# Performance work log

Hardware: AMD Instinct MI355X
Metric: run time of the kernel (lower is better)

## Reference

```python
import jax, jax.numpy as jnp
import numpy as np

B, L, C, H = 256, 256, 512, 512
MOG_ITERS = 5

def _xavier(key, shape):
    fan_in, fan_out = shape[0], shape[1]
    lim = jnp.sqrt(6.0 / (fan_in + fan_out))
    return jax.random.uniform(key, shape, jnp.float32, -lim, lim)

def setup_inputs() -> dict:
    key = jax.random.key(0)
    ks = jax.random.split(key, 7)
    x = jax.random.normal(ks[0], (B, L, C), jnp.float32)
    # Linear weights stored as (in, out); torch Linear computes x @ W.T + b, identical math.
    Wih_w = _xavier(ks[1], (C, 4 * H)); Wih_b = jnp.zeros((4 * H,), jnp.float32)
    Wmx_w = _xavier(ks[2], (C, H));     Wmx_b = jnp.zeros((H,), jnp.float32)
    Wmh_w = _xavier(ks[3], (H, H));     Wmh_b = jnp.zeros((H,), jnp.float32)
    Whm_w = _xavier(ks[4], (H, 4 * H)); Whm_b = jnp.zeros((4 * H,), jnp.float32)
    Q = _xavier(ks[5], (H, C))  # ht @ Q -> (B, C)
    R = _xavier(ks[6], (C, H))  # xt @ R -> (B, H)
    return {"x": x, "Wih_w": Wih_w, "Wih_b": Wih_b, "Wmx_w": Wmx_w, "Wmx_b": Wmx_b,
            "Wmh_w": Wmh_w, "Wmh_b": Wmh_b, "Whm_w": Whm_w, "Whm_b": Whm_b, "Q": Q, "R": R}

def reference(x, Wih_w, Wih_b, Wmx_w, Wmx_b, Wmh_w, Wmh_b, Whm_w, Whm_b, Q, R):
    batch = x.shape[0]
    h0 = jnp.zeros((batch, H), x.dtype)
    c0 = jnp.zeros((batch, H), x.dtype)

    def step(carry, xt):
        ht, Ct = carry
        # Mogrify: odd iters update xt, even iters update ht
        for i in range(1, MOG_ITERS + 1):
            if i % 2 == 0:
                ht = 2.0 * jax.nn.sigmoid(xt @ R) * ht
            else:
                xt = 2.0 * jax.nn.sigmoid(ht @ Q) * xt
        mt = (xt @ Wmx_w + Wmx_b) + (ht @ Wmh_w + Wmh_b)
        gates = (xt @ Wih_w + Wih_b) + (mt @ Whm_w + Whm_b)
        ingate, forgetgate, cellgate, outgate = jnp.split(gates, 4, axis=1)
        ft = jax.nn.sigmoid(forgetgate)
        it = jax.nn.sigmoid(ingate)
        cand = jnp.tanh(cellgate)
        ot = jax.nn.sigmoid(outgate)
        Ct = ft * Ct + it * cand
        ht = ot * jnp.tanh(Ct)
        return (ht, Ct), ht

    xs = jnp.swapaxes(x, 0, 1)  # (L, B, C)
    _, hs = jax.lax.scan(step, (h0, c0), xs)
    return jnp.swapaxes(hs, 0, 1)  # (B, L, H)
```

## Files before the change

### kernel.cpp

```cpp
#include <hip/hip_runtime.h>
#include <hip/hip_bf16.h>
#include <cmath>

typedef __attribute__((ext_vector_type(8))) short short8;
typedef __attribute__((ext_vector_type(4))) float f32x4;
typedef __attribute__((ext_vector_type(2))) float f32x2;
typedef __attribute__((ext_vector_type(4))) unsigned int u32x4;

__device__ inline float bf2f(ushort u) {
    unsigned v = (unsigned)u << 16; float f; __builtin_memcpy(&f, &v, 4); return f;
}
__device__ inline ushort f2bf(float f) {
    __hip_bfloat16 h = __float2bfloat16(f); ushort u; __builtin_memcpy(&u, &h, 2); return u;
}
__device__ inline float sigf(float z) { return 1.f / (1.f + expf(-z)); }

__device__ __forceinline__ void agst32(void* p, unsigned v) {
    __hip_atomic_store((unsigned*)p, v, __ATOMIC_RELAXED, __HIP_MEMORY_SCOPE_AGENT);
}

#define BB 256
#define LL 256
#define HH 512
#define G4 2048

__device__ __forceinline__ unsigned swz(unsigned row, unsigned byteInRow) {
    return (row * 1024u + byteInRow) ^ ((row & 7u) << 4);
}

__device__ __forceinline__ void stage_A16(const ushort* Ag, int r0, ushort* Ast, int tid) {
    const char* src = (const char*)(Ag + (size_t)(r0 + (tid >> 4)) * HH + (tid & 15) * 32);
    u32x4 v0, v1, v2, v3;
    asm volatile(
        "global_load_dwordx4 %0, %4, off sc0 sc1\n\t"
        "global_load_dwordx4 %1, %4, off offset:16 sc0 sc1\n\t"
        "global_load_dwordx4 %2, %4, off offset:32 sc0 sc1\n\t"
        "global_load_dwordx4 %3, %4, off offset:48 sc0 sc1\n\t"
        "s_waitcnt vmcnt(0)"
        : "=&v"(v0), "=&v"(v1), "=&v"(v2), "=&v"(v3) : "v"(src) : "memory");
    unsigned row = (unsigned)(tid >> 4), b = (unsigned)((tid & 15) * 64);
    *(u32x4*)((char*)Ast + swz(row, b))      = v0;
    *(u32x4*)((char*)Ast + swz(row, b + 16)) = v1;
    *(u32x4*)((char*)Ast + swz(row, b + 32)) = v2;
    *(u32x4*)((char*)Ast + swz(row, b + 48)) = v3;
}

__device__ __forceinline__ void rb_arrive(unsigned* slots, int sub, unsigned epoch) {
    asm volatile("s_waitcnt vmcnt(0)" ::: "memory");
    __syncthreads();
    if (threadIdx.x == 0)
        __hip_atomic_store(slots + sub, epoch, __ATOMIC_RELAXED, __HIP_MEMORY_SCOPE_AGENT);
}
__device__ __forceinline__ void rb_wait(unsigned* slots, unsigned epoch) {
    if (threadIdx.x < 16)
        while (__hip_atomic_load(slots + threadIdx.x, __ATOMIC_RELAXED,
                                 __HIP_MEMORY_SCOPE_AGENT) < epoch)
            __builtin_amdgcn_s_sleep(1);
    __syncthreads();
}


__global__ __launch_bounds__(256) void init_state(ushort* hp) {
    int i = blockIdx.x * 256 + threadIdx.x;
    hp[i] = 0;
}

__global__ __launch_bounds__(256) void transpose_f32_bf16(
    const float* __restrict__ in, ushort* __restrict__ out, int K, int N)
{
    __shared__ float tile[32][33];
    int tx = threadIdx.x & 31, ty = threadIdx.x >> 5;
    int bk = blockIdx.x * 32, bn = blockIdx.y * 32;
    #pragma unroll
    for (int i = 0; i < 32; i += 8)
        tile[ty + i][tx] = in[(size_t)(bk + ty + i) * N + (bn + tx)];
    __syncthreads();
    #pragma unroll
    for (int i = 0; i < 32; i += 8)
        out[(size_t)(bn + ty + i) * K + (bk + tx)] = f2bf(tile[tx][ty + i]);
}

__global__ __launch_bounds__(256) void combine_w(
    const float* __restrict__ base, const float* __restrict__ A,
    const float* __restrict__ Bm, float* __restrict__ out, int use_base)
{
    int n  = blockIdx.x * 256 + threadIdx.x;
    int k0 = blockIdx.y * 8;
    float acc[8];
    #pragma unroll
    for (int r = 0; r < 8; ++r)
        acc[r] = use_base ? base[(size_t)(k0 + r) * G4 + n] : 0.f;
    for (int m = 0; m < 512; ++m) {
        float bv = Bm[(size_t)m * G4 + n];
        #pragma unroll
        for (int r = 0; r < 8; ++r)
            acc[r] = fmaf(A[(size_t)(k0 + r) * 512 + m], bv, acc[r]);
    }
    #pragma unroll
    for (int r = 0; r < 8; ++r) out[(size_t)(k0 + r) * G4 + n] = acc[r];
}

__global__ __launch_bounds__(256) void bias_g_kernel(
    const float* __restrict__ Wih_b, const float* __restrict__ Whm_b,
    const float* __restrict__ Wmx_b, const float* __restrict__ Wmh_b,
    const float* __restrict__ Whm, float* __restrict__ bias_g)
{
    int n = blockIdx.x * 256 + threadIdx.x;
    float acc = Wih_b[n] + Whm_b[n];
    for (int m = 0; m < 512; ++m)
        acc = fmaf(Wmx_b[m] + Wmh_b[m], Whm[(size_t)m * G4 + n], acc);
    bias_g[n] = acc;
}


__device__ __forceinline__ void mog_stage_p(
    const ushort* Ast,
    const ushort* Wlds,
    ushort (*myBuf)[32], ushort* __restrict__ outG,
    const float* __restrict__ xscale, float (*pbuf)[16][16],
    int r0, int cs, int t, int tid)
{
    int lane = tid & 63, wave = tid >> 6;
    int lr = lane & 15, lk = lane >> 4;
    int ct = wave & 1, kh = wave >> 1;
    int colloc = ct * 16 + lr;

    float xs[4];
    if (xscale != nullptr && kh == 0) {
        #pragma unroll
        for (int r = 0; r < 4; ++r)
            xs[r] = xscale[((size_t)(r0 + lk * 4 + r) * LL + t) * HH + cs * 32 + colloc];
    }

    f32x4 acc = {0.f, 0.f, 0.f, 0.f};
    #pragma unroll
    for (int kk = 0; kk < 8; ++kk) {
        short8 a = *(const short8*)((const char*)Ast +
                     swz((unsigned)lr, (unsigned)(kh * 512 + kk * 64 + lk * 16)));
        short8 b = *(const short8*)((const char*)Wlds +
                     swz((unsigned)colloc, (unsigned)(kh * 512 + kk * 64 + lk * 16)));
        acc = __builtin_amdgcn_mfma_f32_16x16x32_bf16(a, b, acc, 0, 0, 0);
    }

    if (kh == 1) {
        #pragma unroll
        for (int r = 0; r < 4; ++r) pbuf[ct][lk * 4 + r][lr] = acc[r];
    }
    __syncthreads();
    if (kh == 0) {
        #pragma unroll
        for (int r = 0; r < 4; ++r) {
            float v = acc[r] + pbuf[ct][lk * 4 + r][lr];
            float sc = (xscale != nullptr) ? xs[r] : bf2f(myBuf[lk * 4 + r][colloc]);
            myBuf[lk * 4 + r][colloc] = f2bf(2.f * sigf(v) * sc);
        }
    }
    __syncthreads();
    {
        int row = tid >> 4, c2 = tid & 15;
        unsigned v = *(const unsigned*)&myBuf[row][c2 * 2];
        agst32((char*)outG + (((size_t)(r0 + row)) * HH + cs * 32 + c2 * 2) * 2, v);
    }
}

__global__ __launch_bounds__(256) void moglstm_persistent(
    const float* __restrict__ x,
    const ushort* __restrict__ QT, const ushort* __restrict__ RT,
    const ushort* __restrict__ W1T, const ushort* __restrict__ W2T,
    const float* __restrict__ biasg,
    ushort* __restrict__ hp, ushort* __restrict__ xa, ushort* __restrict__ hb1,
    ushort* __restrict__ xb, ushort* __restrict__ hb2, ushort* __restrict__ xc,
    float* __restrict__ out, unsigned* __restrict__ flags)
{
    __shared__ ushort QTs[32 * 512];
    __shared__ ushort RTs[32 * 512];
    __shared__ ushort Ast[16 * 512];
    __shared__ float  pbuf[2][16][16];
    __shared__ ushort myX[16][32];
    __shared__ ushort myH[16][32];
    __shared__ float  gbuf[4][16][32];

    int tid = threadIdx.x;
    int rb = blockIdx.x >> 4, cs = blockIdx.x & 15;
    int r0 = rb * 16;
    int lane = tid & 63, wave = tid >> 6;
    int lr = lane & 15, lk = lane >> 4;

    #pragma unroll
    for (int i = 0; i < 8; ++i) {
        int ch = i * 256 + tid, col = ch >> 6, kc = ch & 63;
        *(u32x4*)((char*)QTs + swz((unsigned)col, (unsigned)(kc * 16))) =
            *(const u32x4*)(QT + (size_t)(cs * 32 + col) * HH + kc * 8);
        *(u32x4*)((char*)RTs + swz((unsigned)col, (unsigned)(kc * 16))) =
            *(const u32x4*)(RT + (size_t)(cs * 32 + col) * HH + kc * 8);
    }
    ((unsigned*)myH)[tid] = 0;
    float Creg0 = 0.f, Creg1 = 0.f;
    __syncthreads();

    unsigned* slots = flags + rb * 16;

    for (int t = 0; t < LL; ++t) {
        unsigned ep = (unsigned)t * 6u;

        stage_A16(hp, r0, Ast, tid); __syncthreads();
        mog_stage_p(Ast, QTs, myX, xa, x, pbuf, r0, cs, t, tid);
        rb_arrive(slots, cs, ep + 1); rb_wait(slots, ep + 1);
        stage_A16(xa, r0, Ast, tid); __syncthreads();
        mog_stage_p(Ast, RTs, myH, hb1, nullptr, pbuf, r0, cs, t, tid);
        rb_arrive(slots, cs, ep + 2); rb_wait(slots, ep + 2);
        stage_A16(hb1, r0, Ast, tid); __syncthreads();
        mog_stage_p(Ast, QTs, myX, xb, nullptr, pbuf, r0, cs, t, tid);
        rb_arrive(slots, cs, ep + 3); rb_wait(slots, ep + 3);
        stage_A16(xb, r0, Ast, tid); __syncthreads();
        mog_stage_p(Ast, RTs, myH, hb2, nullptr, pbuf, r0, cs, t, tid);
        rb_arrive(slots, cs, ep + 4); rb_wait(slots, ep + 4);

        stage_A16(hb2, r0, Ast, tid); __syncthreads();
        mog_stage_p(Ast, QTs, myX, xc, nullptr, pbuf, r0, cs, t, tid);
        rb_arrive(slots, cs, ep + 5);

        int q = wave;
        f32x4 acc0 = {0,0,0,0}, acc1 = {0,0,0,0};
        {
            const short8* B0 = (const short8*)(W2T + (size_t)(q * 512 + cs * 32 + lr) * HH);
            const short8* B1 = (const short8*)(W2T + (size_t)(q * 512 + cs * 32 + 16 + lr) * HH);
            #pragma unroll
            for (int kk = 0; kk < 16; ++kk) {
                short8 a = *(const short8*)((const char*)Ast +
                             swz((unsigned)lr, (unsigned)(kk * 64 + lk * 16)));
                acc0 = __builtin_amdgcn_mfma_f32_16x16x32_bf16(a, B0[kk * 4 + lk], acc0, 0, 0, 0);
                acc1 = __builtin_amdgcn_mfma_f32_16x16x32_bf16(a, B1[kk * 4 + lk], acc1, 0, 0, 0);
            }
        }
        rb_wait(slots, ep + 5);

        stage_A16(xc, r0, Ast, tid); __syncthreads();
        {
            const short8* B0 = (const short8*)(W1T + (size_t)(q * 512 + cs * 32 + lr) * HH);
            const short8* B1 = (const short8*)(W1T + (size_t)(q * 512 + cs * 32 + 16 + lr) * HH);
            #pragma unroll
            for (int kk = 0; kk < 16; ++kk) {
                short8 a = *(const short8*)((const char*)Ast +
                             swz((unsigned)lr, (unsigned)(kk * 64 + lk * 16)));
                acc0 = __builtin_amdgcn_mfma_f32_16x16x32_bf16(a, B0[kk * 4 + lk], acc0, 0, 0, 0);
                acc1 = __builtin_amdgcn_mfma_f32_16x16x32_bf16(a, B1[kk * 4 + lk], acc1, 0, 0, 0);
            }
        }
        {
            float b0 = biasg[q * 512 + cs * 32 + lr];
            float b1 = biasg[q * 512 + cs * 32 + 16 + lr];
            #pragma unroll
            for (int r = 0; r < 4; ++r) {
                gbuf[q][lk * 4 + r][lr]      = acc0[r] + b0;
                gbuf[q][lk * 4 + r][16 + lr] = acc1[r] + b1;
            }
        }
        __syncthreads();
        {
            int row = tid >> 4, c2 = tid & 15;
            int colg = cs * 32 + c2 * 2;
            float i0 = sigf(gbuf[0][row][c2 * 2]),      f0 = sigf(gbuf[1][row][c2 * 2]);
            float g0 = tanhf(gbuf[2][row][c2 * 2]),     o0 = sigf(gbuf[3][row][c2 * 2]);
            Creg0 = f0 * Creg0 + i0 * g0;
            float h0v = o0 * tanhf(Creg0);
            float i1 = sigf(gbuf[0][row][c2 * 2 + 1]),  f1 = sigf(gbuf[1][row][c2 * 2 + 1]);
            float g1 = tanhf(gbuf[2][row][c2 * 2 + 1]), o1 = sigf(gbuf[3][row][c2 * 2 + 1]);
            Creg1 = f1 * Creg1 + i1 * g1;
            float h1v = o1 * tanhf(Creg1);
            f32x2 hv2 = {h0v, h1v};
            *(f32x2*)(out + ((size_t)(r0 + row) * LL + t) * HH + colg) = hv2;
            unsigned hu = (unsigned)f2bf(h0v) | ((unsigned)f2bf(h1v) << 16);
            agst32((char*)hp + (((size_t)(r0 + row)) * HH + colg) * 2, hu);
            *(unsigned*)&myH[row][c2 * 2] = hu;
        }
        rb_arrive(slots, cs, ep + 6); rb_wait(slots, ep + 6);
    }
}

extern "C" void kernel_launch(void* const* d_in, const int* in_sizes, int n_in,
                              void* d_out, int out_size, void* d_ws, size_t ws_size,
                              hipStream_t stream)
{
    const float* x     = (const float*)d_in[0];
    const float* Wih_w = (const float*)d_in[1];
    const float* Wih_b = (const float*)d_in[2];
    const float* Wmx_w = (const float*)d_in[3];
    const float* Wmx_b = (const float*)d_in[4];
    const float* Wmh_w = (const float*)d_in[5];
    const float* Wmh_b = (const float*)d_in[6];
    const float* Whm_w = (const float*)d_in[7];
    const float* Whm_b = (const float*)d_in[8];
    const float* Q     = (const float*)d_in[9];
    const float* R     = (const float*)d_in[10];
    float* out = (float*)d_out;

    char* ws = (char*)d_ws;
    ushort* QT   = (ushort*)ws;               ws += (size_t)512 * 512 * 2;
    ushort* RT   = (ushort*)ws;               ws += (size_t)512 * 512 * 2;
    ushort* W1T  = (ushort*)ws;               ws += (size_t)G4  * 512 * 2;
    ushort* W2T  = (ushort*)ws;               ws += (size_t)G4  * 512 * 2;
    float*  biasg= (float*)ws;                ws += (size_t)G4 * 4;
    ushort* xa   = (ushort*)ws;               ws += (size_t)BB * HH * 2;
    ushort* hb1  = (ushort*)ws;               ws += (size_t)BB * HH * 2;
    ushort* xb   = (ushort*)ws;               ws += (size_t)BB * HH * 2;
    ushort* hb2  = (ushort*)ws;               ws += (size_t)BB * HH * 2;
    ushort* xc   = (ushort*)ws;               ws += (size_t)BB * HH * 2;
    ushort* hp   = (ushort*)ws;               ws += (size_t)BB * HH * 2;
    float*  Wtmp = (float*)ws;                ws += (size_t)512 * G4 * 4;

    unsigned* flags = (unsigned*)Wtmp;

    init_state<<<512, 256, 0, stream>>>(hp);
    transpose_f32_bf16<<<dim3(16, 16), 256, 0, stream>>>(Q, QT, 512, 512);
    transpose_f32_bf16<<<dim3(16, 16), 256, 0, stream>>>(R, RT, 512, 512);
    combine_w<<<dim3(8, 64), 256, 0, stream>>>(Wih_w, Wmx_w, Whm_w, Wtmp, 1);
    transpose_f32_bf16<<<dim3(16, 64), 256, 0, stream>>>(Wtmp, W1T, 512, G4);
    combine_w<<<dim3(8, 64), 256, 0, stream>>>(nullptr, Wmh_w, Whm_w, Wtmp, 0);
    transpose_f32_bf16<<<dim3(16, 64), 256, 0, stream>>>(Wtmp, W2T, 512, G4);
    bias_g_kernel<<<8, 256, 0, stream>>>(Wih_b, Whm_b, Wmx_b, Wmh_b, Whm_w, biasg);
    hipMemsetAsync(flags, 0, (size_t)16 * 16 * sizeof(unsigned), stream);

    moglstm_persistent<<<256, 256, 0, stream>>>(x, QT, RT, W1T, W2T, biasg,
                                                hp, xa, hb1, xb, hb2, xc, out, flags);
}
```

Measured before the change: 7.258 ms.

## Replace block-wide barriers with per-wave flags and per-slice polling

Swaps the row-block barrier for per-wave epoch flags. Before, one thread published a block flag after a __syncthreads and 16 threads polled every peer before a second __syncthreads. Now each wave publishes its own flag once its stores drain, and each lane polls only the four wave flags of the producer block whose slice it is about to load. This removes a block barrier and all-to-all waiting from each of the six dependent stages per timestep. The cost is four times as many flags and more polling traffic, plus a risk of LDS reuse hazards where the removed barriers used to order Ast reads and writes.

```diff
diff --git a/kernel.cpp b/kernel.cpp
--- a/kernel.cpp
+++ b/kernel.cpp
@@ -28,8 +28,24 @@
     return (row * 1024u + byteInRow) ^ ((row & 7u) << 4);
 }
 
-__device__ __forceinline__ void stage_A16(const ushort* Ag, int r0, ushort* Ast, int tid) {
-    const char* src = (const char*)(Ag + (size_t)(r0 + (tid >> 4)) * HH + (tid & 15) * 32);
+__device__ __forceinline__ void arrive_wave(unsigned* fl, int cs, unsigned epoch, int tid) {
+    asm volatile("s_waitcnt vmcnt(0)" ::: "memory");
+    if ((tid & 63) == 0)
+        __hip_atomic_store(fl + cs * 4 + (tid >> 6), epoch,
+                           __ATOMIC_RELAXED, __HIP_MEMORY_SCOPE_AGENT);
+}
+
+__device__ __forceinline__ void stage_poll(
+    const ushort* __restrict__ Ag, int r0, ushort* Ast,
+    unsigned* __restrict__ fl, unsigned epoch, int tid)
+{
+    int w = tid >> 6, l = tid & 63;
+    int p = 4 * w + (l >> 4);
+    int row = l & 15;
+    unsigned* myf = fl + p * 4 + (l & 3);
+    while (__hip_atomic_load(myf, __ATOMIC_RELAXED, __HIP_MEMORY_SCOPE_AGENT) < epoch)
+        __builtin_amdgcn_s_sleep(1);
+    const char* src = (const char*)(Ag + (size_t)(r0 + row) * HH + p * 32);
     u32x4 v0, v1, v2, v3;
     asm volatile(
         "global_load_dwordx4 %0, %4, off sc0 sc1\n\t"
@@ -38,25 +54,11 @@
         "global_load_dwordx4 %3, %4, off offset:48 sc0 sc1\n\t"
         "s_waitcnt vmcnt(0)"
         : "=&v"(v0), "=&v"(v1), "=&v"(v2), "=&v"(v3) : "v"(src) : "memory");
-    unsigned row = (unsigned)(tid >> 4), b = (unsigned)((tid & 15) * 64);
-    *(u32x4*)((char*)Ast + swz(row, b))      = v0;
-    *(u32x4*)((char*)Ast + swz(row, b + 16)) = v1;
-    *(u32x4*)((char*)Ast + swz(row, b + 32)) = v2;
-    *(u32x4*)((char*)Ast + swz(row, b + 48)) = v3;
-}
-
-__device__ __forceinline__ void rb_arrive(unsigned* slots, int sub, unsigned epoch) {
-    asm volatile("s_waitcnt vmcnt(0)" ::: "memory");
-    __syncthreads();
-    if (threadIdx.x == 0)
-        __hip_atomic_store(slots + sub, epoch, __ATOMIC_RELAXED, __HIP_MEMORY_SCOPE_AGENT);
-}
-__device__ __forceinline__ void rb_wait(unsigned* slots, unsigned epoch) {
-    if (threadIdx.x < 16)
-        while (__hip_atomic_load(slots + threadIdx.x, __ATOMIC_RELAXED,
-                                 __HIP_MEMORY_SCOPE_AGENT) < epoch)
-            __builtin_amdgcn_s_sleep(1);
-    __syncthreads();
+    unsigned b = (unsigned)(p * 64);
+    *(u32x4*)((char*)Ast + swz((unsigned)row, b))      = v0;
+    *(u32x4*)((char*)Ast + swz((unsigned)row, b + 16)) = v1;
+    *(u32x4*)((char*)Ast + swz((unsigned)row, b + 32)) = v2;
+    *(u32x4*)((char*)Ast + swz((unsigned)row, b + 48)) = v3;
 }
 
 
@@ -113,9 +115,8 @@
 }
 
 
-__device__ __forceinline__ void mog_stage_p(
-    const ushort* Ast,
-    const ushort* Wlds,
+__device__ __forceinline__ void mog_compute(
+    const ushort* Ast, const ushort* Wlds,
     ushort (*myBuf)[32], ushort* __restrict__ outG,
     const float* __restrict__ xscale, float (*pbuf)[16][16],
     int r0, int cs, int t, int tid)
@@ -198,27 +199,26 @@
     float Creg0 = 0.f, Creg1 = 0.f;
     __syncthreads();
 
-    unsigned* slots = flags + rb * 16;
+    unsigned* fl = flags + rb * 64;
 
     for (int t = 0; t < LL; ++t) {
         unsigned ep = (unsigned)t * 6u;
 
-        stage_A16(hp, r0, Ast, tid); __syncthreads();
-        mog_stage_p(Ast, QTs, myX, xa, x, pbuf, r0, cs, t, tid);
-        rb_arrive(slots, cs, ep + 1); rb_wait(slots, ep + 1);
-        stage_A16(xa, r0, Ast, tid); __syncthreads();
-        mog_stage_p(Ast, RTs, myH, hb1, nullptr, pbuf, r0, cs, t, tid);
-        rb_arrive(slots, cs, ep + 2); rb_wait(slots, ep + 2);
-        stage_A16(hb1, r0, Ast, tid); __syncthreads();
-        mog_stage_p(Ast, QTs, myX, xb, nullptr, pbuf, r0, cs, t, tid);
-        rb_arrive(slots, cs, ep + 3); rb_wait(slots, ep + 3);
-        stage_A16(xb, r0, Ast, tid); __syncthreads();
-        mog_stage_p(Ast, RTs, myH, hb2, nullptr, pbuf, r0, cs, t, tid);
-        rb_arrive(slots, cs, ep + 4); rb_wait(slots, ep + 4);
-
-        stage_A16(hb2, r0, Ast, tid); __syncthreads();
-        mog_stage_p(Ast, QTs, myX, xc, nullptr, pbuf, r0, cs, t, tid);
-        rb_arrive(slots, cs, ep + 5);
+        stage_poll(hp, r0, Ast, fl, ep, tid); __syncthreads();
+        mog_compute(Ast, QTs, myX, xa, x, pbuf, r0, cs, t, tid);
+        arrive_wave(fl, cs, ep + 1, tid);
+        stage_poll(xa, r0, Ast, fl, ep + 1, tid); __syncthreads();
+        mog_compute(Ast, RTs, myH, hb1, nullptr, pbuf, r0, cs, t, tid);
+        arrive_wave(fl, cs, ep + 2, tid);
+        stage_poll(hb1, r0, Ast, fl, ep + 2, tid); __syncthreads();
+        mog_compute(Ast, QTs, myX, xb, nullptr, pbuf, r0, cs, t, tid);
+        arrive_wave(fl, cs, ep + 3, tid);
+        stage_poll(xb, r0, Ast, fl, ep + 3, tid); __syncthreads();
+        mog_compute(Ast, RTs, myH, hb2, nullptr, pbuf, r0, cs, t, tid);
+        arrive_wave(fl, cs, ep + 4, tid);
+        stage_poll(hb2, r0, Ast, fl, ep + 4, tid); __syncthreads();
+        mog_compute(Ast, QTs, myX, xc, nullptr, pbuf, r0, cs, t, tid);
+        arrive_wave(fl, cs, ep + 5, tid);
 
         int q = wave;
         f32x4 acc0 = {0,0,0,0}, acc1 = {0,0,0,0};
@@ -233,9 +233,8 @@
                 acc1 = __builtin_amdgcn_mfma_f32_16x16x32_bf16(a, B1[kk * 4 + lk], acc1, 0, 0, 0);
             }
         }
-        rb_wait(slots, ep + 5);
-
-        stage_A16(xc, r0, Ast, tid); __syncthreads();
+        __syncthreads();
+        stage_poll(xc, r0, Ast, fl, ep + 5, tid); __syncthreads();
         {
             const short8* B0 = (const short8*)(W1T + (size_t)(q * 512 + cs * 32 + lr) * HH);
             const short8* B1 = (const short8*)(W1T + (size_t)(q * 512 + cs * 32 + 16 + lr) * HH);
@@ -274,7 +273,7 @@
             agst32((char*)hp + (((size_t)(r0 + row)) * HH + colg) * 2, hu);
             *(unsigned*)&myH[row][c2 * 2] = hu;
         }
-        rb_arrive(slots, cs, ep + 6); rb_wait(slots, ep + 6);
+        arrive_wave(fl, cs, ep + 6, tid);
     }
 }
 
@@ -319,7 +318,7 @@
     combine_w<<<dim3(8, 64), 256, 0, stream>>>(nullptr, Wmh_w, Whm_w, Wtmp, 0);
     transpose_f32_bf16<<<dim3(16, 64), 256, 0, stream>>>(Wtmp, W2T, 512, G4);
     bias_g_kernel<<<8, 256, 0, stream>>>(Wih_b, Whm_b, Wmx_b, Wmh_b, Whm_w, biasg);
-    hipMemsetAsync(flags, 0, (size_t)16 * 16 * sizeof(unsigned), stream);
+    hipMemsetAsync(flags, 0, (size_t)16 * 64 * sizeof(unsigned), stream);
 
     moglstm_persistent<<<256, 256, 0, stream>>>(x, QT, RT, W1T, W2T, biasg,
                                                 hp, xa, hb1, xb, hb2, xc, out, flags);
```

Result: slower. 8.143 ms (+12.2%).
